# Kernel tuning notes

Hardware: AMD Instinct MI355X
Metric: run time of the kernel (lower is better)

## Reference

```python
import jax, jax.numpy as jnp
import numpy as np

N, E, B = 100000, 1600000, 64
TD, VD, AD = 768, 2048, 512
HC, H = 32, 4
NV, NA = 20000, 20000


def setup_inputs() -> dict:
    key = jax.random.key(0)
    ks = iter(jax.random.split(key, 80))
    def nrm(shape, scale=0.05):
        return (jax.random.normal(next(ks), shape, jnp.float32) * scale)
    inp = {}
    inp["x"] = jax.random.normal(next(ks), (N, TD), jnp.float32)
    inp["x_vision"] = jax.random.normal(next(ks), (NV, VD), jnp.float32)
    inp["x_audio"] = jax.random.normal(next(ks), (NA, AD), jnp.float32)
    inp["src"] = jax.random.randint(next(ks), (E,), 0, N, jnp.int32)
    inp["dst"] = jax.random.randint(next(ks), (E,), 0, N, jnp.int32)
    inp["vidx"] = jnp.arange(NV, dtype=jnp.int32) + 1000   # disjoint vision node ids
    inp["aidx"] = jnp.arange(NA, dtype=jnp.int32) + 30000  # disjoint audio node ids
    inp["ptr"] = (jnp.arange(B + 1) * (N // B)).astype(jnp.int32)
    # modality projections
    inp["Wt"] = nrm((HC, TD)); inp["bt"] = jnp.zeros((HC,), jnp.float32)
    inp["Wv"] = nrm((HC, VD)); inp["bv"] = jnp.zeros((HC,), jnp.float32)
    inp["gv"] = jnp.ones((HC,), jnp.float32); inp["bev"] = jnp.zeros((HC,), jnp.float32)
    inp["Wa"] = nrm((HC, AD)); inp["ba"] = jnp.zeros((HC,), jnp.float32)
    inp["ga"] = jnp.ones((HC,), jnp.float32); inp["bea"] = jnp.zeros((HC,), jnp.float32)
    # GATv2 convs: (in_dim, heads, concat)
    for p, cin, h, concat in (("c1", HC, H, True), ("c2", HC * H, H, True), ("c3", HC * H, H, True), ("c4", HC * H, 1, False)):
        inp[p + "_Wl"] = nrm((h * HC, cin)); inp[p + "_bl"] = jnp.zeros((h * HC,), jnp.float32)
        inp[p + "_Wr"] = nrm((h * HC, cin)); inp[p + "_br"] = jnp.zeros((h * HC,), jnp.float32)
        inp[p + "_att"] = nrm((h, HC))
        inp[p + "_b"] = jnp.zeros((h * HC if concat else HC,), jnp.float32)
    # layer norms
    for p, d in (("n1", HC * H), ("n2", HC * H), ("n3", HC * H), ("n4", HC)):
        inp[p + "_g"] = jnp.ones((d,), jnp.float32); inp[p + "_b"] = jnp.zeros((d,), jnp.float32)
    inp["Wo"] = nrm((1, HC), 0.01); inp["bo"] = jnp.zeros((1,), jnp.float32)
    return inp


def layernorm(x, g, b):
    m = x.mean(-1, keepdims=True)
    v = x.var(-1, keepdims=True)
    return (x - m) / jnp.sqrt(v + 1e-5) * g + b


def gatv2(x, src, dst, Wl, bl, Wr, br, att, b, concat):
    # PyG GATv2Conv (share_weights=False): e = att . leaky_relu(xl[src] + xr[dst])
    n = x.shape[0]
    h, c = att.shape
    xl = (x @ Wl.T + bl).reshape(n, h, c)
    xr = (x @ Wr.T + br).reshape(n, h, c)
    e = jnp.einsum('ehc,hc->eh', jax.nn.leaky_relu(xl[src] + xr[dst], 0.2), att)
    m = jax.ops.segment_max(e, dst, num_segments=n)          # segment softmax over dst
    w = jnp.exp(e - m[dst])
    s = jax.ops.segment_sum(w, dst, num_segments=n)
    alpha = w / (s[dst] + 1e-16)
    out = jax.ops.segment_sum(alpha[:, :, None] * xl[src], dst, num_segments=n)
    out = out.reshape(n, h * c) if concat else out.mean(1)
    return out + b


def reference(x, x_vision, x_audio, Wt, bt, Wv, bv, gv, bev, Wa, ba, ga, bea,
              c1_Wl, c1_bl, c1_Wr, c1_br, c1_att, c1_b,
              c2_Wl, c2_bl, c2_Wr, c2_br, c2_att, c2_b,
              c3_Wl, c3_bl, c3_Wr, c3_br, c3_att, c3_b,
              c4_Wl, c4_bl, c4_Wr, c4_br, c4_att, c4_b,
              n1_g, n1_b, n2_g, n2_b, n3_g, n3_b, n4_g, n4_b, Wo, bo,
              src, dst, vidx, aidx, ptr):
    n = x.shape[0]
    sl = jnp.arange(n, dtype=src.dtype)  # add_self_loops=True
    s2 = jnp.concatenate([src, sl]); d2 = jnp.concatenate([dst, sl])
    fx = x @ Wt.T + bt  # text projection (dropout = identity in eval)
    hv = jax.nn.relu(layernorm(x_vision @ Wv.T + bv, gv, bev))
    fx = fx.at[vidx].set(hv * x[vidx].mean(1, keepdims=True))
    ha = jax.nn.relu(layernorm(x_audio @ Wa.T + ba, ga, bea))
    fx = fx.at[aidx].set(ha * x[aidx].mean(1, keepdims=True))
    h1 = jax.nn.elu(layernorm(gatv2(fx, s2, d2, c1_Wl, c1_bl, c1_Wr, c1_br, c1_att, c1_b, True), n1_g, n1_b))
    h2 = jax.nn.elu(layernorm(gatv2(h1, s2, d2, c2_Wl, c2_bl, c2_Wr, c2_br, c2_att, c2_b, True) + h1, n2_g, n2_b))
    h3 = jax.nn.elu(layernorm(gatv2(h2, s2, d2, c3_Wl, c3_bl, c3_Wr, c3_br, c3_att, c3_b, True) + h2, n3_g, n3_b))
    h4 = layernorm(gatv2(h3, s2, d2, c4_Wl, c4_bl, c4_Wr, c4_br, c4_att, c4_b, False), n4_g, n4_b)
    summary = h4[ptr[:-1]]  # summary node = first node of each graph
    out = (summary @ Wo.T + bo).squeeze(-1)  # num_classes==2 -> squeeze
    return out
```

## Files before the change

kernel.cpp:

```cpp
#include <hip/hip_runtime.h>
#include <math.h>

#define NND 100000
#define NED 1600000
#define TDIM 768
#define VDIM 2048
#define ADIM 512
#define NVV 20000
#define NAA 20000
#define NBB 64
#define SUBROWS 8192

#define NBLK_N ((NND + 255) / 256)
#define NBLK_E ((NED + 255) / 256)
#define NSCAN ((NND + 1023) / 1024)
#define NPACK 576
#define NT_TXT ((NND + 63) / 64)
#define NT_VIS ((NVV + 63) / 64)
#define NT_AUD ((NAA + 63) / 64)

static __device__ __forceinline__ unsigned short f2bf(float f) {
  unsigned int u = __float_as_uint(f);
  unsigned int r = (u + 0x7fffu + ((u >> 16) & 1u)) >> 16;
  return (unsigned short)r;
}
static __device__ __forceinline__ float bf2f(unsigned int s) {
  return __uint_as_float(s << 16);
}

typedef __attribute__((ext_vector_type(8))) short bfrag;
typedef __attribute__((ext_vector_type(4))) float facc4;

static __device__ __forceinline__ bfrag pack8(const float4& a, const float4& b) {
  union { bfrag v; unsigned short u[8]; } r;
  r.u[0] = f2bf(a.x); r.u[1] = f2bf(a.y); r.u[2] = f2bf(a.z); r.u[3] = f2bf(a.w);
  r.u[4] = f2bf(b.x); r.u[5] = f2bf(b.y); r.u[6] = f2bf(b.z); r.u[7] = f2bf(b.w);
  return r.v;
}

static __device__ __forceinline__ float red16(float v) {
  #pragma unroll
  for (int m = 8; m >= 1; m >>= 1) v += __shfl_xor(v, m, 64);
  return v;
}
static __device__ __forceinline__ float red32(float v) {
  #pragma unroll
  for (int m = 16; m >= 1; m >>= 1) v += __shfl_xor(v, m, 64);
  return v;
}

__global__ void k_init(int* cnt, int* fill, int* m3, int* m2, int* cnts, int* agg, int n) {
  int i = blockIdx.x * 256 + threadIdx.x;
  if (i < n) { cnt[i] = 1; fill[i] = 1; m3[i] = 0; m2[i] = 0; }
  if (i < 2) cnts[i] = 0;
  if (i < 128) agg[i] = 0;
}

__global__ void k_cntpack(
    const int* __restrict__ dst, int* cnt,
    const float* __restrict__ W0l, const float* __restrict__ W0r, unsigned short* o0,
    const float* __restrict__ W1l, const float* __restrict__ W1r, unsigned short* o1,
    const float* __restrict__ W2l, const float* __restrict__ W2r, unsigned short* o2,
    const float* __restrict__ W3l, const float* __restrict__ W3r, unsigned short* o3,
    const float* __restrict__ Wt, unsigned short* ot,
    const float* __restrict__ Wv, unsigned short* ov,
    const float* __restrict__ Wa, unsigned short* oa) {
  int bid = blockIdx.x;
  if (bid < NBLK_E) {
    int i = bid * 256 + threadIdx.x;
    if (i < NED) atomicAdd(&cnt[dst[i]], 1);
    return;
  }
  int i = (bid - NBLK_E) * 256 + threadIdx.x;
  if (i < 4096) { o0[i] = f2bf(W0l[i]); o0[4096 + i] = f2bf(W0r[i]); return; }
  i -= 4096;
  if (i < 16384) { o1[i] = f2bf(W1l[i]); o1[16384 + i] = f2bf(W1r[i]); return; }
  i -= 16384;
  if (i < 16384) { o2[i] = f2bf(W2l[i]); o2[16384 + i] = f2bf(W2r[i]); return; }
  i -= 16384;
  if (i < 4096) { o3[i] = f2bf(W3l[i]); o3[4096 + i] = f2bf(W3r[i]); return; }
  i -= 4096;
  if (i < 24576) { ot[i] = f2bf(Wt[i]); return; }
  i -= 24576;
  if (i < 65536) { ov[i] = f2bf(Wv[i]); return; }
  i -= 65536;
  if (i < 16384) { oa[i] = f2bf(Wa[i]); return; }
}

__global__ void k_scanall(const int* __restrict__ cnt, int* rp, int* agg, int n) {
  __shared__ int lds[256];
  int t = threadIdx.x, b = blockIdx.x;
  int base = b * 1024;
  int v[4];
  int s = 0;
  #pragma unroll
  for (int j = 0; j < 4; ++j) {
    int i = base + t * 4 + j;
    int c = (i < n) ? cnt[i] : 0;
    s += c; v[j] = s;
  }
  lds[t] = s;
  __syncthreads();
  for (int ofs = 1; ofs < 256; ofs <<= 1) {
    int x = (t >= ofs) ? lds[t - ofs] : 0;
    __syncthreads();
    lds[t] += x;
    __syncthreads();
  }
  int excl = (t > 0) ? lds[t - 1] : 0;
  int total = lds[255];
  if (t == 0) atomicExch(&agg[b], total);
  __syncthreads();
  int psum = 0;
  for (int j = t; j < b; j += 256) {
    int a;
    do { a = atomicAdd(&agg[j], 0); } while (a == 0);
    psum += a;
  }
  lds[t] = psum;
  __syncthreads();
  for (int ofs = 128; ofs >= 1; ofs >>= 1) {
    if (t < ofs) lds[t] += lds[t + ofs];
    __syncthreads();
  }
  int prefix = lds[0];
  #pragma unroll
  for (int j = 0; j < 4; ++j) {
    int i = base + t * 4 + j;
    if (i < n) rp[i + 1] = prefix + excl + v[j];
  }
  if (b == 0 && t == 0) rp[0] = 0;
}

__global__ void k_fill(const int* __restrict__ src, const int* __restrict__ dst,
                       const int* __restrict__ rp, int* fill, int* colidx, int n, int e) {
  int i = blockIdx.x * 256 + threadIdx.x;
  if (i < n) colidx[rp[i]] = i;
  if (i < e) {
    int d = dst[i];
    int p = atomicAdd(&fill[d], 1);
    colidx[rp[d] + p] = src[i];
  }
}

__global__ void k_prep4m(const int* __restrict__ ptr, const int* __restrict__ rp,
                         const int* __restrict__ colidx, int* off, int* gidx, int* mark3) {
  if (blockIdx.x > 0) {
    int node = ptr[blockIdx.x - 1];
    int eb = rp[node], ee = rp[node + 1];
    if (threadIdx.x == 0) mark3[node] = 1;
    for (int e = eb + (int)threadIdx.x; e < ee; e += 256) mark3[colidx[e]] = 1;
    return;
  }
  __shared__ int cnt_s[64];
  __shared__ int off_s[65];
  int t = threadIdx.x;
  if (t < 64) {
    int node = ptr[t];
    int deg = rp[node + 1] - rp[node];
    if (deg > 126) deg = 126;
    cnt_s[t] = deg + 1;
  }
  __syncthreads();
  if (t == 0) {
    int acc = 0;
    for (int i = 0; i < 64; ++i) { off_s[i] = acc; acc += cnt_s[i]; }
    off_s[64] = acc;
  }
  __syncthreads();
  if (t < 65) off[t] = off_s[t];
  if (t < 64) {
    int node = ptr[t];
    int o = off_s[t];
    gidx[o] = node;
    int eb = rp[node];
    int deg = cnt_s[t] - 1;
    for (int j = 0; j < deg; ++j) gidx[o + 1 + j] = colidx[eb + j];
  }
}

__global__ void k_mark2s(const int* __restrict__ mark3, const int* __restrict__ rp,
                         const int* __restrict__ colidx, int* mark2, int n) {
  int i = blockIdx.x * 256 + threadIdx.x;
  if (i >= n || !mark3[i]) return;
  mark2[i] = 1;
  int eb = rp[i], ee = rp[i + 1];
  for (int e = eb; e < ee; ++e) mark2[colidx[e]] = 1;
}

__global__ void k_compact2(const int* __restrict__ m3, const int* __restrict__ m2,
                           int* l3, int* l2, int* cnts, int n) {
  int i = blockIdx.x * 256 + threadIdx.x;
  if (i < n) {
    if (m3[i]) { int p = atomicAdd(&cnts[0], 1); l3[p] = i; }
    if (m2[i]) { int p = atomicAdd(&cnts[1], 1); l2[p] = i; }
  }
}

template <int K, bool MEAN, bool OBF>
static __device__ __forceinline__ void gemm_in_body(
    const float* __restrict__ A, const unsigned short* __restrict__ Wb,
    const float* __restrict__ bias, void* __restrict__ Cv,
    float* __restrict__ rowmean, int M, int bid) {
  constexpr int KT = K / 32;
  const int wid = (int)threadIdx.x >> 6;
  const int lane = (int)threadIdx.x & 63;
  const int r16 = lane & 15;
  const int kg = lane >> 4;
  const int m0 = (bid * 4 + wid) * 16;
  if (m0 >= M) return;
  const float* arow = A + (size_t)(m0 + r16) * K + kg * 8;
  const unsigned short* w0 = Wb + (size_t)r16 * K + kg * 8;
  const unsigned short* w1 = Wb + (size_t)(16 + r16) * K + kg * 8;
  facc4 acc0 = (facc4){0.f, 0.f, 0.f, 0.f};
  facc4 acc1 = (facc4){0.f, 0.f, 0.f, 0.f};
  float msum = 0.f;
  #pragma unroll 4
  for (int kt = 0; kt < KT; ++kt) {
    const float4* ap = reinterpret_cast<const float4*>(arow + kt * 32);
    float4 a0 = ap[0], a1 = ap[1];
    if (MEAN) msum += (a0.x + a0.y + a0.z + a0.w) + (a1.x + a1.y + a1.z + a1.w);
    bfrag af = pack8(a0, a1);
    bfrag b0 = *reinterpret_cast<const bfrag*>(w0 + kt * 32);
    bfrag b1 = *reinterpret_cast<const bfrag*>(w1 + kt * 32);
    acc0 = __builtin_amdgcn_mfma_f32_16x16x32_bf16(af, b0, acc0, 0, 0, 0);
    acc1 = __builtin_amdgcn_mfma_f32_16x16x32_bf16(af, b1, acc1, 0, 0, 0);
  }
  float b0v = bias[r16], b1v = bias[16 + r16];
  #pragma unroll
  for (int r = 0; r < 4; ++r) {
    int rowg = m0 + kg * 4 + r;
    float v0 = acc0[r] + b0v, v1 = acc1[r] + b1v;
    if (OBF) {
      unsigned short* C = (unsigned short*)Cv;
      C[(size_t)rowg * 32 + r16] = f2bf(v0);
      C[(size_t)rowg * 32 + 16 + r16] = f2bf(v1);
    } else {
      float* C = (float*)Cv;
      C[(size_t)rowg * 32 + r16] = v0;
      C[(size_t)rowg * 32 + 16 + r16] = v1;
    }
  }
  if (MEAN) {
    msum += __shfl_xor(msum, 16, 64);
    msum += __shfl_xor(msum, 32, 64);
    if (lane < 16) rowmean[m0 + r16] = msum * (1.f / (float)K);
  }
}

__global__ __launch_bounds__(256) void k_gemm_in_all(
    const float* __restrict__ x, const unsigned short* __restrict__ wbt,
    const float* __restrict__ bt, unsigned short* fx, float* rowmean,
    const float* __restrict__ xv, const unsigned short* __restrict__ wbv,
    const float* __restrict__ bv, float* hvraw,
    const float* __restrict__ xa, const unsigned short* __restrict__ wba,
    const float* __restrict__ ba, float* haraw) {
  int bid = blockIdx.x;
  if (bid < NT_TXT) {
    gemm_in_body<TDIM, true, true>(x, wbt, bt, fx, rowmean, NND, bid);
  } else if (bid < NT_TXT + NT_VIS) {
    gemm_in_body<VDIM, false, false>(xv, wbv, bv, hvraw, nullptr, NVV, bid - NT_TXT);
  } else {
    gemm_in_body<ADIM, false, false>(xa, wba, ba, haraw, nullptr, NAA, bid - NT_TXT - NT_VIS);
  }
}

template <int K, int NHALF, int WAVES, int MODE>
__global__ __launch_bounds__(WAVES * 64) void gemm_mfma(
    const unsigned short* __restrict__ A,
    const unsigned short* __restrict__ Wb,
    const float* __restrict__ bl, const float* __restrict__ br,
    unsigned short* __restrict__ Cl, unsigned short* __restrict__ Cr, int M,
    const int* __restrict__ rows, const int* __restrict__ rcnt) {
  constexpr int KT = K / 32;
  constexpr int NT = 2 * NHALF / 16;
  constexpr int NPW = NT / WAVES;
  static_assert(NPW >= 1, "bad wave split");
  const int wid = (int)threadIdx.x >> 6;
  const int lane = (int)threadIdx.x & 63;
  const int r16 = lane & 15;
  const int kg = lane >> 4;
  const int m0 = blockIdx.x * 16;
  int nr = M;
  if (MODE >= 1) nr = *rcnt;
  if (m0 >= nr) return;
  bfrag bf[NPW][KT];
  #pragma unroll
  for (int n = 0; n < NPW; ++n) {
    int col = (wid * NPW + n) * 16 + r16;
    #pragma unroll
    for (int kt = 0; kt < KT; ++kt)
      bf[n][kt] = *reinterpret_cast<const bfrag*>(Wb + (size_t)col * K + kt * 32 + kg * 8);
  }
  int ra = m0 + r16;
  if (MODE >= 1) { int mm = ra < nr ? ra : nr - 1; ra = rows[mm]; }
  bfrag af[KT];
  const unsigned short* arow = A + (size_t)ra * K + kg * 8;
  #pragma unroll
  for (int kt = 0; kt < KT; ++kt)
    af[kt] = *reinterpret_cast<const bfrag*>(arow + kt * 32);
  facc4 acc[NPW];
  #pragma unroll
  for (int n = 0; n < NPW; ++n) acc[n] = (facc4){0.f, 0.f, 0.f, 0.f};
  #pragma unroll
  for (int kt = 0; kt < KT; ++kt)
    #pragma unroll
    for (int n = 0; n < NPW; ++n)
      acc[n] = __builtin_amdgcn_mfma_f32_16x16x32_bf16(af[kt], bf[n][kt], acc[n], 0, 0, 0);
  #pragma unroll
  for (int n = 0; n < NPW; ++n) {
    int colg = (wid * NPW + n) * 16 + r16;
    bool isL = colg < NHALF;
    float bias = isL ? bl[colg] : br[colg - NHALF];
    #pragma unroll
    for (int r = 0; r < 4; ++r) {
      int m = m0 + kg * 4 + r;
      if (MODE == 1 && m >= nr) continue;
      int rowg = (MODE == 1) ? rows[m] : m;
      unsigned short v = f2bf(acc[n][r] + bias);
      if (isL) Cl[(size_t)rowg * NHALF + colg] = v;
      else     Cr[(size_t)rowg * NHALF + (colg - NHALF)] = v;
    }
  }
}

template <bool RES, bool WL>
__global__ __launch_bounds__(256) void gat_agg_post128(
    const unsigned short* __restrict__ xl, const unsigned short* __restrict__ xr,
    const float* __restrict__ att,
    const int* __restrict__ rp, const int* __restrict__ colidx,
    const float* __restrict__ cb, const unsigned short* res,
    const float* __restrict__ g, const float* __restrict__ b,
    unsigned short* __restrict__ out, int n,
    const int* __restrict__ wl, const int* __restrict__ wcnt) {
  int wid = (blockIdx.x * 256 + threadIdx.x) >> 6;
  int node;
  if (WL) {
    if (wid >= *wcnt) return;
    node = wl[wid];
  } else {
    if (wid >= n) return;
    node = wid;
  }
  const int base = node * 128;
  int l = threadIdx.x & 63;
  const int lh = l & 31;
  const int half = l >> 5;
  const int c4 = 4 * lh;
  float4 a = *reinterpret_cast<const float4*>(att + c4);
  uint2 xru = *reinterpret_cast<const uint2*>(xr + base + c4);
  float xr0 = bf2f(xru.x & 0xffffu), xr1 = bf2f(xru.x >> 16);
  float xr2 = bf2f(xru.y & 0xffffu), xr3 = bf2f(xru.y >> 16);
  float m_ = -1e30f, s_ = 0.f;
  float ac0 = 0.f, ac1 = 0.f, ac2 = 0.f, ac3 = 0.f;
  int eb = rp[node], ee = rp[node + 1];
  int cnt = ee - eb;
  int nstep = (cnt + 1) >> 1;

  auto step = [&](uint2 cur, bool go) {
    float x0 = bf2f(cur.x & 0xffffu), x1 = bf2f(cur.x >> 16);
    float x2 = bf2f(cur.y & 0xffffu), x3 = bf2f(cur.y >> 16);
    float z0 = x0 + xr0, z1 = x1 + xr1, z2 = x2 + xr2, z3 = x3 + xr3;
    float t = (z0 > 0.f ? z0 : 0.2f * z0) * a.x + (z1 > 0.f ? z1 : 0.2f * z1) * a.y
            + (z2 > 0.f ? z2 : 0.2f * z2) * a.z + (z3 > 0.f ? z3 : 0.2f * z3) * a.w;
    t += __shfl_xor(t, 1, 64);
    t += __shfl_xor(t, 2, 64);
    t += __shfl_xor(t, 4, 64);
    if (!go) t = -1e30f;
    if (__any(t > m_ + 4.0f)) {
      float nm = fmaxf(m_, t);
      float p = __expf(m_ - nm);
      float w = __expf(t - nm);
      s_ = s_ * p + w;
      ac0 = ac0 * p + w * x0; ac1 = ac1 * p + w * x1;
      ac2 = ac2 * p + w * x2; ac3 = ac3 * p + w * x3;
      m_ = nm;
    } else {
      float w = __expf(t - m_);
      s_ += w;
      ac0 = fmaf(w, x0, ac0); ac1 = fmaf(w, x1, ac1);
      ac2 = fmaf(w, x2, ac2); ac3 = fmaf(w, x3, ac3);
    }
  };
  auto eclamp = [&](int s) { int e = 2 * s + half; return eb + (e < cnt ? e : cnt - 1); };
  auto ldx = [&](int sn) {
    return *reinterpret_cast<const uint2*>(xl + (size_t)sn * 128 + c4);
  };

  int idx[4];
  uint2 pv[4];
  #pragma unroll
  for (int k = 0; k < 4; ++k) idx[k] = colidx[eclamp(k)];
  #pragma unroll
  for (int k = 0; k < 4; ++k) pv[k] = ldx(idx[k]);
  for (int i = 0; i < nstep; i += 4) {
    uint2 q[4];
    #pragma unroll
    for (int k = 0; k < 4; ++k) q[k] = pv[k];
    if (i + 4 < nstep) {
      #pragma unroll
      for (int k = 0; k < 4; ++k) idx[k] = colidx[eclamp(i + 4 + k)];
      #pragma unroll
      for (int k = 0; k < 4; ++k) pv[k] = ldx(idx[k]);
    }
    step(q[0], 2 * i + half < cnt);
    if (i + 1 < nstep) step(q[1], 2 * (i + 1) + half < cnt);
    if (i + 2 < nstep) step(q[2], 2 * (i + 2) + half < cnt);
    if (i + 3 < nstep) step(q[3], 2 * (i + 3) + half < cnt);
  }

  float om = __shfl_xor(m_, 32, 64);
  float os = __shfl_xor(s_, 32, 64);
  float oa0 = __shfl_xor(ac0, 32, 64);
  float oa1 = __shfl_xor(ac1, 32, 64);
  float oa2 = __shfl_xor(ac2, 32, 64);
  float oa3 = __shfl_xor(ac3, 32, 64);
  float nm = fmaxf(m_, om);
  float ps = __expf(m_ - nm), po = __expf(om - nm);
  float s = s_ * ps + os * po;
  float inv = 1.f / (s + 1e-16f);
  float4 cbv = *reinterpret_cast<const float4*>(cb + c4);
  float v0 = (ac0 * ps + oa0 * po) * inv + cbv.x;
  float v1 = (ac1 * ps + oa1 * po) * inv + cbv.y;
  float v2 = (ac2 * ps + oa2 * po) * inv + cbv.z;
  float v3 = (ac3 * ps + oa3 * po) * inv + cbv.w;
  if (RES) {
    uint2 rv = *reinterpret_cast<const uint2*>(res + base + c4);
    v0 += bf2f(rv.x & 0xffffu); v1 += bf2f(rv.x >> 16);
    v2 += bf2f(rv.y & 0xffffu); v3 += bf2f(rv.y >> 16);
  }
  float S = v0 + v1 + v2 + v3;
  float Q = v0 * v0 + v1 * v1 + v2 * v2 + v3 * v3;
  #pragma unroll
  for (int m = 16; m >= 1; m >>= 1) {
    S += __shfl_xor(S, m, 64);
    Q += __shfl_xor(Q, m, 64);
  }
  float mean = S * (1.f / 128.f);
  float var = Q * (1.f / 128.f) - mean * mean;
  float rstd = rsqrtf(var + 1e-5f);
  float4 gv = *reinterpret_cast<const float4*>(g + c4);
  float4 bv = *reinterpret_cast<const float4*>(b + c4);
  float y0 = (v0 - mean) * rstd * gv.x + bv.x;
  float y1 = (v1 - mean) * rstd * gv.y + bv.y;
  float y2 = (v2 - mean) * rstd * gv.z + bv.z;
  float y3 = (v3 - mean) * rstd * gv.w + bv.w;
  y0 = (y0 > 0.f) ? y0 : expm1f(y0);
  y1 = (y1 > 0.f) ? y1 : expm1f(y1);
  y2 = (y2 > 0.f) ? y2 : expm1f(y2);
  y3 = (y3 > 0.f) ? y3 : expm1f(y3);
  if (half == 0) {
    uint2 o;
    o.x = (unsigned int)f2bf(y0) | ((unsigned int)f2bf(y1) << 16);
    o.y = (unsigned int)f2bf(y2) | ((unsigned int)f2bf(y3) << 16);
    *reinterpret_cast<uint2*>(out + base + c4) = o;
  }
}

__global__ __launch_bounds__(256) void k_agg4_final(
    const unsigned short* __restrict__ xls, const unsigned short* __restrict__ xrs,
    const float* __restrict__ att, const int* __restrict__ off,
    const float* __restrict__ cb, const float* __restrict__ g,
    const float* __restrict__ b, const float* __restrict__ Wo,
    const float* __restrict__ bo, float* __restrict__ out) {
  int wid = (blockIdx.x * 256 + threadIdx.x) >> 6;
  int l = threadIdx.x & 63;
  int lg = l & 15;
  int node = 4 * wid + (l >> 4);
  int c2 = 2 * lg;
  int p0 = off[node], pe = off[node + 1];
  int deg = pe - p0 - 1;
  float2 a = *reinterpret_cast<const float2*>(att + c2);
  unsigned int xru = *reinterpret_cast<const unsigned int*>(xrs + (size_t)p0 * 32 + c2);
  float xr0 = bf2f(xru & 0xffffu), xr1 = bf2f(xru >> 16);
  float m_ = -1e30f, s_ = 0.f, accx = 0.f, accy = 0.f;
  for (int i = 0;; ++i) {
    bool go = i < deg;
    if (!__any(go)) break;
    float xcx = 0.f, xcy = 0.f;
    float t = -1e30f;
    if (go) {
      unsigned int pv = *reinterpret_cast<const unsigned int*>(xls + (size_t)(p0 + 1 + i) * 32 + c2);
      xcx = bf2f(pv & 0xffffu);
      xcy = bf2f(pv >> 16);
      float z0 = xcx + xr0, z1 = xcy + xr1;
      t = (z0 > 0.f ? z0 : 0.2f * z0) * a.x + (z1 > 0.f ? z1 : 0.2f * z1) * a.y;
    }
    t = red16(t);
    if (!go) t = -1e30f;
    if (__any(t > m_ + 4.0f)) {
      float nm = fmaxf(m_, t);
      float p = __expf(m_ - nm);
      float w = __expf(t - nm);
      s_ = s_ * p + w;
      accx = accx * p + w * xcx;
      accy = accy * p + w * xcy;
      m_ = nm;
    } else {
      float w = __expf(t - m_);
      s_ += w;
      accx = fmaf(w, xcx, accx);
      accy = fmaf(w, xcy, accy);
    }
  }
  float inv = 1.f / (s_ + 1e-16f);
  float2 cbv = *reinterpret_cast<const float2*>(cb + c2);
  float v0 = accx * inv + cbv.x;
  float v1 = accy * inv + cbv.y;
  float S = red16(v0 + v1);
  float Q = red16(v0 * v0 + v1 * v1);
  float mean = S * (1.f / 32.f);
  float var = Q * (1.f / 32.f) - mean * mean;
  float rstd = rsqrtf(var + 1e-5f);
  float2 gv = *reinterpret_cast<const float2*>(g + c2);
  float2 bv = *reinterpret_cast<const float2*>(b + c2);
  float y0 = (v0 - mean) * rstd * gv.x + bv.x;
  float y1 = (v1 - mean) * rstd * gv.y + bv.y;
  float2 wo = *reinterpret_cast<const float2*>(Wo + c2);
  float d = red16(y0 * wo.x + y1 * wo.y);
  if (lg == 0) out[node] = d + bo[0];
}

__global__ __launch_bounds__(256) void k_modal2(
    unsigned short* fx, const float* __restrict__ hv, const float* __restrict__ ha,
    const int* __restrict__ vidx, const int* __restrict__ aidx,
    const float* __restrict__ gv, const float* __restrict__ bev,
    const float* __restrict__ ga, const float* __restrict__ bea,
    const float* __restrict__ rowmean, int nv, int na) {
  int wid = (blockIdx.x * 256 + threadIdx.x) >> 6;
  int l = threadIdx.x & 63;
  if (wid >= nv + na) return;
  bool isV = wid < nv;
  int w2 = isV ? wid : wid - nv;
  const float* hraw = isV ? hv : ha;
  const float* gg = isV ? gv : ga;
  const float* be = isV ? bev : bea;
  int node = isV ? vidx[w2] : aidx[w2];
  float mean = rowmean[node];
  float hval = (l < 32) ? hraw[(size_t)w2 * 32 + l] : 0.f;
  float S = red32(hval);
  float Q = red32(hval * hval);
  if (l < 32) {
    float m2 = S * (1.f / 32.f);
    float var = Q * (1.f / 32.f) - m2 * m2;
    float rstd = rsqrtf(var + 1e-5f);
    float y = (hval - m2) * rstd * gg[l] + be[l];
    y = fmaxf(y, 0.f);
    fx[(size_t)node * 32 + l] = f2bf(y * mean);
  }
}

extern "C" void kernel_launch(void* const* d_in, const int* in_sizes, int n_in,
                              void* d_out, int out_size, void* d_ws, size_t ws_size,
                              hipStream_t stream) {
  const float* x   = (const float*)d_in[0];
  const float* xv  = (const float*)d_in[1];
  const float* xa  = (const float*)d_in[2];
  const int* src   = (const int*)d_in[3];
  const int* dst   = (const int*)d_in[4];
  const int* vidx  = (const int*)d_in[5];
  const int* aidx  = (const int*)d_in[6];
  const int* ptr   = (const int*)d_in[7];
  const float* Wt  = (const float*)d_in[8];
  const float* bt  = (const float*)d_in[9];
  const float* Wv  = (const float*)d_in[10];
  const float* bv  = (const float*)d_in[11];
  const float* gv  = (const float*)d_in[12];
  const float* bev = (const float*)d_in[13];
  const float* Wa  = (const float*)d_in[14];
  const float* ba  = (const float*)d_in[15];
  const float* ga  = (const float*)d_in[16];
  const float* bea = (const float*)d_in[17];
  const float* cW_l[4], *cb_l[4], *cW_r[4], *cb_r[4], *c_att[4], *c_b[4];
  for (int i = 0; i < 4; ++i) {
    cW_l[i]  = (const float*)d_in[18 + 6 * i + 0];
    cb_l[i]  = (const float*)d_in[18 + 6 * i + 1];
    cW_r[i]  = (const float*)d_in[18 + 6 * i + 2];
    cb_r[i]  = (const float*)d_in[18 + 6 * i + 3];
    c_att[i] = (const float*)d_in[18 + 6 * i + 4];
    c_b[i]   = (const float*)d_in[18 + 6 * i + 5];
  }
  const float* ng[4], *nb_[4];
  for (int i = 0; i < 4; ++i) {
    ng[i]  = (const float*)d_in[42 + 2 * i + 0];
    nb_[i] = (const float*)d_in[42 + 2 * i + 1];
  }
  const float* Wo = (const float*)d_in[50];
  const float* bo = (const float*)d_in[51];
  float* out = (float*)d_out;

  char* w = (char*)d_ws;
  auto alloc = [&](size_t bytes) {
    char* p = w;
    w += (bytes + 255) & ~(size_t)255;
    return p;
  };
  int* rowptr = (int*)alloc((NND + 1) * sizeof(int));
  int* cnt    = (int*)alloc(NND * sizeof(int));
  int* aggs   = (int*)alloc(128 * sizeof(int));
  int* colidx = (int*)alloc((size_t)(NED + NND) * sizeof(int));
  float* rowmean = (float*)alloc((size_t)NND * sizeof(float));
  unsigned short* fx = (unsigned short*)alloc((size_t)NND * 32 * sizeof(unsigned short));
  unsigned short* h  = (unsigned short*)alloc((size_t)NND * 128 * sizeof(unsigned short));
  unsigned short* xlb = (unsigned short*)alloc((size_t)NND * 128 * sizeof(unsigned short));
  unsigned short* xrb = (unsigned short*)alloc((size_t)NND * 128 * sizeof(unsigned short));
  float* hvraw = (float*)alloc((size_t)NVV * 32 * sizeof(float));
  float* haraw = (float*)alloc((size_t)NAA * 32 * sizeof(float));
  unsigned short* wb0 = (unsigned short*)alloc(256 * 32 * sizeof(unsigned short));
  unsigned short* wb1 = (unsigned short*)alloc(256 * 128 * sizeof(unsigned short));
  unsigned short* wb2 = (unsigned short*)alloc(256 * 128 * sizeof(unsigned short));
  unsigned short* wb3 = (unsigned short*)alloc(64 * 128 * sizeof(unsigned short));
  unsigned short* wbt = (unsigned short*)alloc(32 * TDIM * sizeof(unsigned short));
  unsigned short* wbv = (unsigned short*)alloc(32 * VDIM * sizeof(unsigned short));
  unsigned short* wba = (unsigned short*)alloc(32 * ADIM * sizeof(unsigned short));
  int* off4 = (int*)alloc(65 * sizeof(int));
  int* gidx = (int*)alloc(SUBROWS * sizeof(int));
  unsigned short* xls = (unsigned short*)alloc((size_t)SUBROWS * 32 * sizeof(unsigned short));
  unsigned short* xrs = (unsigned short*)alloc((size_t)SUBROWS * 32 * sizeof(unsigned short));
  int* mark3 = (int*)alloc((size_t)NND * sizeof(int));
  int* mark2 = (int*)alloc((size_t)NND * sizeof(int));
  int* list3 = (int*)alloc((size_t)NND * sizeof(int));
  int* list2 = (int*)alloc((size_t)NND * sizeof(int));
  int* cnts  = (int*)alloc(2 * sizeof(int));

  const int nwave_n = (NND * 64 + 255) / 256;
  const int nwave_m2 = ((NVV + NAA) * 64 + 255) / 256;
  const int ntile = (NND + 15) / 16;

  int* fill = list2;
  k_init<<<NBLK_N, 256, 0, stream>>>(cnt, fill, mark3, mark2, cnts, aggs, NND);
  k_cntpack<<<NBLK_E + NPACK, 256, 0, stream>>>(
      dst, cnt,
      cW_l[0], cW_r[0], wb0, cW_l[1], cW_r[1], wb1,
      cW_l[2], cW_r[2], wb2, cW_l[3], cW_r[3], wb3,
      Wt, wbt, Wv, wbv, Wa, wba);
  k_scanall<<<NSCAN, 256, 0, stream>>>(cnt, rowptr, aggs, NND);
  k_fill<<<NBLK_E, 256, 0, stream>>>(src, dst, rowptr, fill, colidx, NND, NED);
  k_prep4m<<<65, 256, 0, stream>>>(ptr, rowptr, colidx, off4, gidx, mark3);
  k_mark2s<<<NBLK_N, 256, 0, stream>>>(mark3, rowptr, colidx, mark2, NND);
  k_compact2<<<NBLK_N, 256, 0, stream>>>(mark3, mark2, list3, list2, cnts, NND);
  k_gemm_in_all<<<NT_TXT + NT_VIS + NT_AUD, 256, 0, stream>>>(
      x, wbt, bt, fx, rowmean, xv, wbv, bv, hvraw, xa, wba, ba, haraw);
  k_modal2<<<nwave_m2, 256, 0, stream>>>(
      fx, hvraw, haraw, vidx, aidx, gv, bev, ga, bea, rowmean, NVV, NAA);

  gemm_mfma<32, 128, 8, 0><<<ntile, 512, 0, stream>>>(
      fx, wb0, cb_l[0], cb_r[0], xlb, xrb, NND, nullptr, nullptr);
  gat_agg_post128<false, false><<<nwave_n, 256, 0, stream>>>(
      xlb, xrb, c_att[0], rowptr, colidx, c_b[0], nullptr, ng[0], nb_[0], h, NND,
      nullptr, nullptr);

  gemm_mfma<128, 128, 8, 0><<<ntile, 512, 0, stream>>>(
      h, wb1, cb_l[1], cb_r[1], xlb, xrb, NND, nullptr, nullptr);
  gat_agg_post128<true, true><<<nwave_n, 256, 0, stream>>>(
      xlb, xrb, c_att[1], rowptr, colidx, c_b[1], h, ng[1], nb_[1], h, NND,
      list2, cnts + 1);

  gemm_mfma<128, 128, 8, 1><<<ntile, 512, 0, stream>>>(
      h, wb2, cb_l[2], cb_r[2], xlb, xrb, NND, list2, cnts + 1);
  gat_agg_post128<true, true><<<4096, 256, 0, stream>>>(
      xlb, xrb, c_att[2], rowptr, colidx, c_b[2], h, ng[2], nb_[2], h, NND,
      list3, cnts + 0);

  gemm_mfma<128, 32, 4, 2><<<SUBROWS / 16, 256, 0, stream>>>(
      h, wb3, cb_l[3], cb_r[3], xls, xrs, SUBROWS, gidx, off4 + 64);
  k_agg4_final<<<4, 256, 0, stream>>>(
      xls, xrs, c_att[3], off4, c_b[3], ng[3], nb_[3], Wo, bo, out);
}
```

Measured before the change: 629.4 us.

## Software-pipeline input-projection GEMM with async global-to-LDS loads and weight ring

The input projection GEMM now streams activation tiles through a 4-deep per-wave LDS ring using global_load_lds. Weight fragments are prefetched in a 4-slot register ring, and manual vmcnt waits keep several K-steps of loads in flight while MFMAs run on earlier data. This targets the latency-bound, memory-heavy streaming of the large x/x_vision/x_audio matrices. The cost is 32 KB of shared memory per block, which may reduce occupancy, and hand-counted waitcnt values that must match the real instruction count for correctness.

```diff
diff --git a/kernel.cpp b/kernel.cpp
--- a/kernel.cpp
+++ b/kernel.cpp
@@ -36,6 +36,12 @@
   r.u[0] = f2bf(a.x); r.u[1] = f2bf(a.y); r.u[2] = f2bf(a.z); r.u[3] = f2bf(a.w);
   r.u[4] = f2bf(b.x); r.u[5] = f2bf(b.y); r.u[6] = f2bf(b.z); r.u[7] = f2bf(b.w);
   return r.v;
+}
+
+typedef __attribute__((address_space(1))) const unsigned int gas1_t;
+typedef __attribute__((address_space(3))) unsigned int las3_t;
+static __device__ __forceinline__ void gld_lds16(const void* g, void* l) {
+  __builtin_amdgcn_global_load_lds((gas1_t*)g, (las3_t*)l, 16, 0, 0);
 }
 
 static __device__ __forceinline__ float red16(float v) {
@@ -201,31 +207,71 @@
 static __device__ __forceinline__ void gemm_in_body(
     const float* __restrict__ A, const unsigned short* __restrict__ Wb,
     const float* __restrict__ bias, void* __restrict__ Cv,
-    float* __restrict__ rowmean, int M, int bid) {
+    float* __restrict__ rowmean, int M, int bid, char* smem_wave) {
   constexpr int KT = K / 32;
+  static_assert(KT % 4 == 0 && KT >= 8, "KT must be multiple of 4, >= 8");
   const int wid = (int)threadIdx.x >> 6;
   const int lane = (int)threadIdx.x & 63;
   const int r16 = lane & 15;
   const int kg = lane >> 4;
   const int m0 = (bid * 4 + wid) * 16;
   if (m0 >= M) return;
-  const float* arow = A + (size_t)(m0 + r16) * K + kg * 8;
+  const float* gsrc = A + (size_t)(m0 + r16) * K + kg * 8;
   const unsigned short* w0 = Wb + (size_t)r16 * K + kg * 8;
   const unsigned short* w1 = Wb + (size_t)(16 + r16) * K + kg * 8;
+
+  auto stage = [&](int kt, int slot) {
+    const float* g0 = gsrc + kt * 32;
+    char* l0 = smem_wave + slot * 2048;
+    gld_lds16(g0, l0);
+    gld_lds16(g0 + 4, l0 + 1024);
+  };
+  const float4* rb = reinterpret_cast<const float4*>(smem_wave) + lane;
+
   facc4 acc0 = (facc4){0.f, 0.f, 0.f, 0.f};
   facc4 acc1 = (facc4){0.f, 0.f, 0.f, 0.f};
   float msum = 0.f;
-  #pragma unroll 4
-  for (int kt = 0; kt < KT; ++kt) {
-    const float4* ap = reinterpret_cast<const float4*>(arow + kt * 32);
-    float4 a0 = ap[0], a1 = ap[1];
+  bfrag wring[4][2];
+
+  #pragma unroll
+  for (int p = 0; p < 4; ++p) {
+    stage(p, p);
+    wring[p][0] = *reinterpret_cast<const bfrag*>(w0 + p * 32);
+    wring[p][1] = *reinterpret_cast<const bfrag*>(w1 + p * 32);
+  }
+  for (int kt0 = 0; kt0 < KT - 4; kt0 += 4) {
+    #pragma unroll
+    for (int j = 0; j < 4; ++j) {
+      const int kt = kt0 + j;
+      asm volatile("s_waitcnt vmcnt(14)" ::: "memory");
+      __builtin_amdgcn_sched_barrier(0);
+      float4 a0 = rb[j * 128];
+      float4 a1 = rb[j * 128 + 64];
+      if (MEAN) msum += (a0.x + a0.y + a0.z + a0.w) + (a1.x + a1.y + a1.z + a1.w);
+      bfrag af = pack8(a0, a1);
+      acc0 = __builtin_amdgcn_mfma_f32_16x16x32_bf16(af, wring[j][0], acc0, 0, 0, 0);
+      acc1 = __builtin_amdgcn_mfma_f32_16x16x32_bf16(af, wring[j][1], acc1, 0, 0, 0);
+      __builtin_amdgcn_sched_barrier(0);
+      stage(kt + 4, j);
+      wring[j][0] = *reinterpret_cast<const bfrag*>(w0 + (kt + 4) * 32);
+      wring[j][1] = *reinterpret_cast<const bfrag*>(w1 + (kt + 4) * 32);
+    }
+  }
+  #pragma unroll
+  for (int j = 0; j < 4; ++j) {
+    if (j == 0) asm volatile("s_waitcnt vmcnt(14)" ::: "memory");
+    else if (j == 1) asm volatile("s_waitcnt vmcnt(10)" ::: "memory");
+    else if (j == 2) asm volatile("s_waitcnt vmcnt(6)" ::: "memory");
+    else asm volatile("s_waitcnt vmcnt(2)" ::: "memory");
+    __builtin_amdgcn_sched_barrier(0);
+    float4 a0 = rb[j * 128];
+    float4 a1 = rb[j * 128 + 64];
     if (MEAN) msum += (a0.x + a0.y + a0.z + a0.w) + (a1.x + a1.y + a1.z + a1.w);
     bfrag af = pack8(a0, a1);
-    bfrag b0 = *reinterpret_cast<const bfrag*>(w0 + kt * 32);
-    bfrag b1 = *reinterpret_cast<const bfrag*>(w1 + kt * 32);
-    acc0 = __builtin_amdgcn_mfma_f32_16x16x32_bf16(af, b0, acc0, 0, 0, 0);
-    acc1 = __builtin_amdgcn_mfma_f32_16x16x32_bf16(af, b1, acc1, 0, 0, 0);
-  }
+    acc0 = __builtin_amdgcn_mfma_f32_16x16x32_bf16(af, wring[j][0], acc0, 0, 0, 0);
+    acc1 = __builtin_amdgcn_mfma_f32_16x16x32_bf16(af, wring[j][1], acc1, 0, 0, 0);
+  }
+
   float b0v = bias[r16], b1v = bias[16 + r16];
   #pragma unroll
   for (int r = 0; r < 4; ++r) {
@@ -255,13 +301,15 @@
     const float* __restrict__ bv, float* hvraw,
     const float* __restrict__ xa, const unsigned short* __restrict__ wba,
     const float* __restrict__ ba, float* haraw) {
+  __shared__ char smem[4 * 4 * 2048];
+  char* smem_wave = smem + ((threadIdx.x >> 6) * 4 * 2048);
   int bid = blockIdx.x;
   if (bid < NT_TXT) {
-    gemm_in_body<TDIM, true, true>(x, wbt, bt, fx, rowmean, NND, bid);
+    gemm_in_body<TDIM, true, true>(x, wbt, bt, fx, rowmean, NND, bid, smem_wave);
   } else if (bid < NT_TXT + NT_VIS) {
-    gemm_in_body<VDIM, false, false>(xv, wbv, bv, hvraw, nullptr, NVV, bid - NT_TXT);
+    gemm_in_body<VDIM, false, false>(xv, wbv, bv, hvraw, nullptr, NVV, bid - NT_TXT, smem_wave);
   } else {
-    gemm_in_body<ADIM, false, false>(xa, wba, ba, haraw, nullptr, NAA, bid - NT_TXT - NT_VIS);
+    gemm_in_body<ADIM, false, false>(xa, wba, ba, haraw, nullptr, NAA, bid - NT_TXT - NT_VIS, smem_wave);
   }
 }
 
```

Result: no change. 637.8 us (+1.3%).
